# Kernel tuning notes

Measured on AMD Instinct MI355X. Metric: run time of the kernel, lower is better.

## Reference

```python
import jax, jax.numpy as jnp
import numpy as np

N_SPECIES = 8192
N_REACTIONS = 2_097_152
NNZ_PER_REACTION = 4  # 2 reactants, 2 products
NNZ = NNZ_PER_REACTION * N_REACTIONS


def setup_inputs() -> dict:
    key = jax.random.key(0)
    ks = jax.random.split(key, 10)
    abundances = jax.random.uniform(ks[0], (N_SPECIES,), jnp.float32, 1e-12, 1e-4)
    temperature = jax.random.uniform(ks[1], (), jnp.float32, 10.0, 300.0)
    cr_rate = jax.random.uniform(ks[2], (), jnp.float32, 1e-17, 1e-15)
    fuv_rate = jax.random.uniform(ks[3], (), jnp.float32, 0.1, 10.0)
    # per-reaction modified-Arrhenius parameters
    alpha = jax.random.uniform(ks[4], (N_REACTIONS,), jnp.float32, 1e-12, 1e-9)
    beta = jax.random.uniform(ks[5], (N_REACTIONS,), jnp.float32, -1.0, 1.0)
    gamma = jax.random.uniform(ks[6], (N_REACTIONS,), jnp.float32, 0.0, 50.0)
    # reaction type: 0 = two-body Arrhenius, 1 = cosmic-ray, 2 = photodissociation
    rtype = jax.random.randint(ks[7], (N_REACTIONS,), 0, 3, dtype=jnp.int32)
    # the two reactant species of each reaction (== argwhere(incidence.T < 0))
    react_species = jax.random.randint(ks[8], (N_REACTIONS, 2), 0, N_SPECIES, dtype=jnp.int32)
    # sparse incidence matrix in COO form: rows = species, cols = reactions
    inc_rows = jax.random.randint(ks[9], (NNZ,), 0, N_SPECIES, dtype=jnp.int32)
    inc_cols = jnp.repeat(jnp.arange(N_REACTIONS, dtype=jnp.int32), NNZ_PER_REACTION)
    # first 2 entries of each reaction consumed (-1), last 2 produced (+1)
    inc_vals = jnp.where(jnp.arange(NNZ) % NNZ_PER_REACTION < 2, -1.0, 1.0).astype(jnp.float32)
    return dict(abundances=abundances, temperature=temperature, cr_rate=cr_rate,
                fuv_rate=fuv_rate, alpha=alpha, beta=beta, gamma=gamma,
                rtype=rtype, react_species=react_species,
                inc_rows=inc_rows, inc_cols=inc_cols, inc_vals=inc_vals,
                n_species=N_SPECIES)


def reference(abundances, temperature, cr_rate, fuv_rate, alpha, beta, gamma,
              rtype, react_species, inc_rows, inc_cols, inc_vals, n_species):
    # 1) batched per-reaction rate evaluation (replaces the Python loop of .at[i].set)
    T = temperature
    k_arr = alpha * (T / 300.0) ** beta * jnp.exp(-gamma / T)      # two-body
    k_cr = alpha * cr_rate                                          # cosmic-ray
    k_fuv = alpha * fuv_rate * jnp.exp(-gamma)                      # photo
    rates = jnp.where(rtype == 0, k_arr, jnp.where(rtype == 1, k_cr, k_fuv))
    # 2) multiply each rate by its reactant abundances (scatter-multiply loop fused)
    rates = rates * abundances[react_species].prod(axis=1)          # [R]
    # 3) sparse incidence @ rates -> per-species dy/dt
    contrib = inc_vals * rates[inc_cols]                            # [NNZ]
    return jax.ops.segment_sum(contrib, inc_rows, num_segments=n_species)
```

## Files before the change

kernel.cpp:

```cpp
#include <hip/hip_runtime.h>


#define NSPEC        8192
#define RPT          4
#define MAIN_BLOCKS  512
#define MAIN_THREADS 1024
#define RED_CHUNK    32
#define RED_SLICES   8

__global__ __launch_bounds__(MAIN_THREADS) void jnet_rates_lds(
    const float* __restrict__ abund,
    const float* __restrict__ temperature,
    const float* __restrict__ cr_rate,
    const float* __restrict__ fuv_rate,
    const float* __restrict__ alp,
    const float* __restrict__ bet,
    const float* __restrict__ gam,
    const int*   __restrict__ rtype,
    const int*   __restrict__ react_species,
    const int*   __restrict__ inc_rows,
    float*       __restrict__ partials,
    int n_reactions)
{
    __shared__ float acc[NSPEC];
    __shared__ float ab[NSPEC];
    const int tid = threadIdx.x;

    const float4 z4 = {0.f, 0.f, 0.f, 0.f};
    for (int i = tid * 4; i < NSPEC; i += MAIN_THREADS * 4) {
        *(float4*)(acc + i) = z4;
        *(float4*)(ab + i)  = *(const float4*)(abund + i);
    }
    __syncthreads();

    const float T    = *temperature;
    const float crr  = *cr_rate;
    const float fuvr = *fuv_rate;
    const float LOG2E = 1.4426950408889634f;
    const float log2T300 = __log2f(T * (1.0f / 300.0f));
    const float invTln2  = LOG2E / T;

    const int base = (blockIdx.x * MAIN_THREADS + tid) * RPT;
    if (base < n_reactions) {
        const float4 a4 = *(const float4*)(alp + base);
        const float4 b4 = *(const float4*)(bet + base);
        const float4 g4 = *(const float4*)(gam + base);
        const int4   t4 = *(const int4*)(rtype + base);
        const int4  rsA = *(const int4*)(react_species + 2 * base);
        const int4  rsB = *(const int4*)(react_species + 2 * base + 4);
        const int4  r0  = *(const int4*)(inc_rows + 4 * base);
        const int4  r1  = *(const int4*)(inc_rows + 4 * base + 4);
        const int4  r2  = *(const int4*)(inc_rows + 4 * base + 8);
        const int4  r3  = *(const int4*)(inc_rows + 4 * base + 12);

        const float al[RPT] = {a4.x, a4.y, a4.z, a4.w};
        const float be[RPT] = {b4.x, b4.y, b4.z, b4.w};
        const float ga[RPT] = {g4.x, g4.y, g4.z, g4.w};
        const int   rt[RPT] = {t4.x, t4.y, t4.z, t4.w};
        const int   s0[RPT] = {rsA.x, rsA.z, rsB.x, rsB.z};
        const int   s1[RPT] = {rsA.y, rsA.w, rsB.y, rsB.w};
        const int4  rw[RPT] = {r0, r1, r2, r3};

        float rate[RPT];
#pragma unroll
        for (int j = 0; j < RPT; ++j) {
            const float karr = exp2f(be[j] * log2T300 - ga[j] * invTln2);
            const float kfuv = fuvr * exp2f(-LOG2E * ga[j]);
            const float k = (rt[j] == 0) ? karr : ((rt[j] == 1) ? crr : kfuv);
            rate[j] = al[j] * k * ab[s0[j]] * ab[s1[j]];
        }

#pragma unroll
        for (int j = 0; j < RPT; ++j) {
            const float r = rate[j];
            unsafeAtomicAdd(acc + rw[j].x, -r);
            unsafeAtomicAdd(acc + rw[j].y, -r);
            unsafeAtomicAdd(acc + rw[j].z,  r);
            unsafeAtomicAdd(acc + rw[j].w,  r);
        }
    }
    __syncthreads();

    float* my = partials + (size_t)blockIdx.x * NSPEC;
    for (int i = tid * 4; i < NSPEC; i += MAIN_THREADS * 4)
        *(float4*)(my + i) = *(const float4*)(acc + i);
}

__global__ __launch_bounds__(256) void jnet_reduce(
    const float* __restrict__ partials, float* __restrict__ out)
{
    const int by = blockIdx.x & (RED_SLICES - 1);
    const int bx = blockIdx.x >> 3;
    const int s  = by * (NSPEC / RED_SLICES) + threadIdx.x * 4;
    const float* p = partials + (size_t)bx * RED_CHUNK * NSPEC + s;

    float4 sum = {0.f, 0.f, 0.f, 0.f};
#pragma unroll 8
    for (int b = 0; b < RED_CHUNK; ++b) {
        const float4 v = *(const float4*)(p + (size_t)b * NSPEC);
        sum.x += v.x; sum.y += v.y; sum.z += v.z; sum.w += v.w;
    }
    unsafeAtomicAdd(out + s + 0, sum.x);
    unsafeAtomicAdd(out + s + 1, sum.y);
    unsafeAtomicAdd(out + s + 2, sum.z);
    unsafeAtomicAdd(out + s + 3, sum.w);
}

__global__ __launch_bounds__(256) void jnet_rhs_direct(
    const float* __restrict__ abund, const float* __restrict__ temperature,
    const float* __restrict__ cr_rate, const float* __restrict__ fuv_rate,
    const float* __restrict__ alp, const float* __restrict__ bet,
    const float* __restrict__ gam, const int* __restrict__ rtype,
    const int* __restrict__ react_species, const int* __restrict__ inc_rows,
    float* __restrict__ out, int n_reactions)
{
    const float T = *temperature, crr = *cr_rate, fuvr = *fuv_rate;
    const float LOG2E = 1.4426950408889634f;
    const float log2T300 = __log2f(T * (1.0f / 300.0f));
    const float invTln2  = LOG2E / T;
    const int base = (blockIdx.x * blockDim.x + threadIdx.x) * RPT;
    if (base >= n_reactions) return;
    const float4 a4 = *(const float4*)(alp + base);
    const float4 b4 = *(const float4*)(bet + base);
    const float4 g4 = *(const float4*)(gam + base);
    const int4   t4 = *(const int4*)(rtype + base);
    const int4  rsA = *(const int4*)(react_species + 2 * base);
    const int4  rsB = *(const int4*)(react_species + 2 * base + 4);
    const float al[RPT] = {a4.x, a4.y, a4.z, a4.w};
    const float be[RPT] = {b4.x, b4.y, b4.z, b4.w};
    const float ga[RPT] = {g4.x, g4.y, g4.z, g4.w};
    const int   rt[RPT] = {t4.x, t4.y, t4.z, t4.w};
    const int   s0[RPT] = {rsA.x, rsA.z, rsB.x, rsB.z};
    const int   s1[RPT] = {rsA.y, rsA.w, rsB.y, rsB.w};
#pragma unroll
    for (int j = 0; j < RPT; ++j) {
        const float karr = exp2f(be[j] * log2T300 - ga[j] * invTln2);
        const float kfuv = fuvr * exp2f(-LOG2E * ga[j]);
        const float k = (rt[j] == 0) ? karr : ((rt[j] == 1) ? crr : kfuv);
        const float r = al[j] * k * abund[s0[j]] * abund[s1[j]];
        const int4 rows = *(const int4*)(inc_rows + 4 * (base + j));
        unsafeAtomicAdd(out + rows.x, -r);
        unsafeAtomicAdd(out + rows.y, -r);
        unsafeAtomicAdd(out + rows.z,  r);
        unsafeAtomicAdd(out + rows.w,  r);
    }
}

extern "C" void kernel_launch(void* const* d_in, const int* in_sizes, int n_in,
                              void* d_out, int out_size, void* d_ws, size_t ws_size,
                              hipStream_t stream) {
    const float* abund   = (const float*)d_in[0];
    const float* temp    = (const float*)d_in[1];
    const float* cr      = (const float*)d_in[2];
    const float* fuv     = (const float*)d_in[3];
    const float* alp     = (const float*)d_in[4];
    const float* bet     = (const float*)d_in[5];
    const float* gam     = (const float*)d_in[6];
    const int*   rtype   = (const int*)d_in[7];
    const int*   rspec   = (const int*)d_in[8];
    const int*   incrows = (const int*)d_in[9];
    float* out = (float*)d_out;
    const int R = in_sizes[4];

    hipMemsetAsync(d_out, 0, (size_t)out_size * sizeof(float), stream);

    const size_t needed = (size_t)MAIN_BLOCKS * NSPEC * sizeof(float);
    if (ws_size >= needed) {
        float* partials = (float*)d_ws;
        hipLaunchKernelGGL(jnet_rates_lds, dim3(MAIN_BLOCKS), dim3(MAIN_THREADS),
                           0, stream, abund, temp, cr, fuv, alp, bet, gam,
                           rtype, rspec, incrows, partials, R);
        hipLaunchKernelGGL(jnet_reduce,
                           dim3((MAIN_BLOCKS / RED_CHUNK) * RED_SLICES), dim3(256),
                           0, stream, partials, out);
    } else {
        const int threads = 256;
        const int blocks  = (R + threads * RPT - 1) / (threads * RPT);
        hipLaunchKernelGGL(jnet_rhs_direct, dim3(blocks), dim3(threads), 0, stream,
                           abund, temp, cr, fuv, alp, bet, gam, rtype, rspec,
                           incrows, out, R);
    }
}
```

Measured before the change: 194.8 us.

## Split rate evaluation and LDS scatter into separate kernels, single exp2 per reaction

Splits the fused kernel into two. A rate kernel loads abundances into LDS and writes per-reaction rates to workspace, and a scatter kernel rereads those rates and does the LDS-atomic incidence accumulation into per-block partials. Each kernel now uses only 32 KB of LDS instead of 64 KB, which may raise occupancy. The rate formula is also rewritten to select the exponent argument first and call exp2f once instead of twice. The cost is an extra 8 MB write plus read of the rates array, and one more kernel launch.

```diff
diff --git a/kernel.cpp b/kernel.cpp
--- a/kernel.cpp
+++ b/kernel.cpp
@@ -8,7 +8,7 @@
 #define RED_CHUNK    32
 #define RED_SLICES   8
 
-__global__ __launch_bounds__(MAIN_THREADS) void jnet_rates_lds(
+__global__ __launch_bounds__(MAIN_THREADS) void jnet_rates(
     const float* __restrict__ abund,
     const float* __restrict__ temperature,
     const float* __restrict__ cr_rate,
@@ -18,19 +18,13 @@
     const float* __restrict__ gam,
     const int*   __restrict__ rtype,
     const int*   __restrict__ react_species,
-    const int*   __restrict__ inc_rows,
-    float*       __restrict__ partials,
+    float*       __restrict__ rates,
     int n_reactions)
 {
-    __shared__ float acc[NSPEC];
     __shared__ float ab[NSPEC];
     const int tid = threadIdx.x;
-
-    const float4 z4 = {0.f, 0.f, 0.f, 0.f};
-    for (int i = tid * 4; i < NSPEC; i += MAIN_THREADS * 4) {
-        *(float4*)(acc + i) = z4;
-        *(float4*)(ab + i)  = *(const float4*)(abund + i);
-    }
+    for (int i = tid * 4; i < NSPEC; i += MAIN_THREADS * 4)
+        *(float4*)(ab + i) = *(const float4*)(abund + i);
     __syncthreads();
 
     const float T    = *temperature;
@@ -41,42 +35,64 @@
     const float invTln2  = LOG2E / T;
 
     const int base = (blockIdx.x * MAIN_THREADS + tid) * RPT;
+    if (base >= n_reactions) return;
+
+    const float4 a4 = *(const float4*)(alp + base);
+    const float4 b4 = *(const float4*)(bet + base);
+    const float4 g4 = *(const float4*)(gam + base);
+    const int4   t4 = *(const int4*)(rtype + base);
+    const int4  rsA = *(const int4*)(react_species + 2 * base);
+    const int4  rsB = *(const int4*)(react_species + 2 * base + 4);
+
+    const float al[RPT] = {a4.x, a4.y, a4.z, a4.w};
+    const float be[RPT] = {b4.x, b4.y, b4.z, b4.w};
+    const float ga[RPT] = {g4.x, g4.y, g4.z, g4.w};
+    const int   rt[RPT] = {t4.x, t4.y, t4.z, t4.w};
+    const int   s0[RPT] = {rsA.x, rsA.z, rsB.x, rsB.z};
+    const int   s1[RPT] = {rsA.y, rsA.w, rsB.y, rsB.w};
+
+    float4 r4;
+    float* rr = (float*)&r4;
+#pragma unroll
+    for (int j = 0; j < RPT; ++j) {
+        const float arg = (rt[j] == 0) ? (be[j] * log2T300 - ga[j] * invTln2)
+                        : ((rt[j] == 1) ? 0.0f : (-LOG2E * ga[j]));
+        const float mul = (rt[j] == 0) ? 1.0f : ((rt[j] == 1) ? crr : fuvr);
+        rr[j] = al[j] * mul * exp2f(arg) * ab[s0[j]] * ab[s1[j]];
+    }
+    *(float4*)(rates + base) = r4;
+}
+
+__global__ __launch_bounds__(MAIN_THREADS) void jnet_scatter(
+    const float* __restrict__ rates,
+    const int*   __restrict__ inc_rows,
+    float*       __restrict__ partials,
+    int n_reactions)
+{
+    __shared__ float acc[NSPEC];
+    const int tid = threadIdx.x;
+    const float4 z4 = {0.f, 0.f, 0.f, 0.f};
+    for (int i = tid * 4; i < NSPEC; i += MAIN_THREADS * 4)
+        *(float4*)(acc + i) = z4;
+    __syncthreads();
+
+    const int base = (blockIdx.x * MAIN_THREADS + tid) * RPT;
     if (base < n_reactions) {
-        const float4 a4 = *(const float4*)(alp + base);
-        const float4 b4 = *(const float4*)(bet + base);
-        const float4 g4 = *(const float4*)(gam + base);
-        const int4   t4 = *(const int4*)(rtype + base);
-        const int4  rsA = *(const int4*)(react_species + 2 * base);
-        const int4  rsB = *(const int4*)(react_species + 2 * base + 4);
-        const int4  r0  = *(const int4*)(inc_rows + 4 * base);
-        const int4  r1  = *(const int4*)(inc_rows + 4 * base + 4);
-        const int4  r2  = *(const int4*)(inc_rows + 4 * base + 8);
-        const int4  r3  = *(const int4*)(inc_rows + 4 * base + 12);
-
-        const float al[RPT] = {a4.x, a4.y, a4.z, a4.w};
-        const float be[RPT] = {b4.x, b4.y, b4.z, b4.w};
-        const float ga[RPT] = {g4.x, g4.y, g4.z, g4.w};
-        const int   rt[RPT] = {t4.x, t4.y, t4.z, t4.w};
-        const int   s0[RPT] = {rsA.x, rsA.z, rsB.x, rsB.z};
-        const int   s1[RPT] = {rsA.y, rsA.w, rsB.y, rsB.w};
-        const int4  rw[RPT] = {r0, r1, r2, r3};
-
-        float rate[RPT];
+        const float4 r4 = *(const float4*)(rates + base);
+        const int4   q0 = *(const int4*)(inc_rows + 4 * base);
+        const int4   q1 = *(const int4*)(inc_rows + 4 * base + 4);
+        const int4   q2 = *(const int4*)(inc_rows + 4 * base + 8);
+        const int4   q3 = *(const int4*)(inc_rows + 4 * base + 12);
+
+        const float rr[RPT] = {r4.x, r4.y, r4.z, r4.w};
+        const int4  qq[RPT] = {q0, q1, q2, q3};
 #pragma unroll
         for (int j = 0; j < RPT; ++j) {
-            const float karr = exp2f(be[j] * log2T300 - ga[j] * invTln2);
-            const float kfuv = fuvr * exp2f(-LOG2E * ga[j]);
-            const float k = (rt[j] == 0) ? karr : ((rt[j] == 1) ? crr : kfuv);
-            rate[j] = al[j] * k * ab[s0[j]] * ab[s1[j]];
-        }
-
-#pragma unroll
-        for (int j = 0; j < RPT; ++j) {
-            const float r = rate[j];
-            unsafeAtomicAdd(acc + rw[j].x, -r);
-            unsafeAtomicAdd(acc + rw[j].y, -r);
-            unsafeAtomicAdd(acc + rw[j].z,  r);
-            unsafeAtomicAdd(acc + rw[j].w,  r);
+            const float r = rr[j];
+            unsafeAtomicAdd(acc + qq[j].x, -r);
+            unsafeAtomicAdd(acc + qq[j].y, -r);
+            unsafeAtomicAdd(acc + qq[j].z,  r);
+            unsafeAtomicAdd(acc + qq[j].w,  r);
         }
     }
     __syncthreads();
@@ -134,10 +150,10 @@
     const int   s1[RPT] = {rsA.y, rsA.w, rsB.y, rsB.w};
 #pragma unroll
     for (int j = 0; j < RPT; ++j) {
-        const float karr = exp2f(be[j] * log2T300 - ga[j] * invTln2);
-        const float kfuv = fuvr * exp2f(-LOG2E * ga[j]);
-        const float k = (rt[j] == 0) ? karr : ((rt[j] == 1) ? crr : kfuv);
-        const float r = al[j] * k * abund[s0[j]] * abund[s1[j]];
+        const float arg = (rt[j] == 0) ? (be[j] * log2T300 - ga[j] * invTln2)
+                        : ((rt[j] == 1) ? 0.0f : (-LOG2E * ga[j]));
+        const float mul = (rt[j] == 0) ? 1.0f : ((rt[j] == 1) ? crr : fuvr);
+        const float r = al[j] * mul * exp2f(arg) * abund[s0[j]] * abund[s1[j]];
         const int4 rows = *(const int4*)(inc_rows + 4 * (base + j));
         unsafeAtomicAdd(out + rows.x, -r);
         unsafeAtomicAdd(out + rows.y, -r);
@@ -164,12 +180,16 @@
 
     hipMemsetAsync(d_out, 0, (size_t)out_size * sizeof(float), stream);
 
-    const size_t needed = (size_t)MAIN_BLOCKS * NSPEC * sizeof(float);
-    if (ws_size >= needed) {
-        float* partials = (float*)d_ws;
-        hipLaunchKernelGGL(jnet_rates_lds, dim3(MAIN_BLOCKS), dim3(MAIN_THREADS),
+    const size_t rates_bytes    = (size_t)R * sizeof(float);
+    const size_t partials_bytes = (size_t)MAIN_BLOCKS * NSPEC * sizeof(float);
+    if (ws_size >= rates_bytes + partials_bytes) {
+        float* rates    = (float*)d_ws;
+        float* partials = (float*)((char*)d_ws + rates_bytes);
+        hipLaunchKernelGGL(jnet_rates, dim3(MAIN_BLOCKS), dim3(MAIN_THREADS),
                            0, stream, abund, temp, cr, fuv, alp, bet, gam,
-                           rtype, rspec, incrows, partials, R);
+                           rtype, rspec, rates, R);
+        hipLaunchKernelGGL(jnet_scatter, dim3(MAIN_BLOCKS), dim3(MAIN_THREADS),
+                           0, stream, rates, incrows, partials, R);
         hipLaunchKernelGGL(jnet_reduce,
                            dim3((MAIN_BLOCKS / RED_CHUNK) * RED_SLICES), dim3(256),
                            0, stream, partials, out);
```

New measurement: 210.6 us. 8.1% more time.
